# Optimization experiments

Hardware: AMD Instinct MI355X
Metric: run time of the kernel (lower is better)

Reference implementation:

```python
import jax, jax.numpy as jnp
import numpy as np

NUM_HEADS = 16


def setup_inputs() -> dict:
    key = jax.random.key(0)
    ks = jax.random.split(key, 4)
    B, C, T, D = 1, 1, 3072, 1024
    s = 1.0 / np.sqrt(D)
    return {
        "x": jax.random.normal(ks[0], (B, C, T, D), dtype=jnp.float32),
        "Wq": jax.random.normal(ks[1], (D, D), dtype=jnp.float32) * s,
        "bq": jnp.zeros((D,), dtype=jnp.float32),
        "Wk": jax.random.normal(ks[2], (D, D), dtype=jnp.float32) * s,
        "bk": jnp.zeros((D,), dtype=jnp.float32),
        "Wv": jax.random.normal(ks[3], (D, D), dtype=jnp.float32) * s,
        "bv": jnp.zeros((D,), dtype=jnp.float32),
        "gamma": jnp.float32(0.5),  # learned scalar; 0.0 at torch init, nonzero here for a meaningful signal
    }


def reference(x, Wq, bq, Wk, bk, Wv, bv, gamma):
    # x: (B, C, T, D); Linear acts on last dim (torch: y = x @ W.T + b)
    B, C, T, D = x.shape
    H = NUM_HEADS
    q = (jnp.einsum("bctd,ed->bcte", x, Wq) + bq).reshape(B, -1, T, H)  # (B, X, T, H), X = C*D/H
    k = (jnp.einsum("bctd,ed->bcte", x, Wk) + bk).reshape(B, -1, T, H)
    v = (jnp.einsum("bctd,ed->bcte", x, Wv) + bv).reshape(B, -1, T, H)
    q = q.transpose(0, 3, 2, 1)  # (B, H, T, X)
    k = k.transpose(0, 3, 1, 2)  # (B, H, X, T)
    energy = q @ k               # (B, H, T, T)  -- note: NO 1/sqrt(d) scaling, as in source
    attn = jax.nn.softmax(energy, axis=-1)
    v = v.transpose(0, 3, 2, 1)  # (B, H, T, X)
    out = attn @ v               # (B, H, T, X)
    out = out.transpose(0, 2, 3, 1).reshape(B, T, -1)  # (B, T, X*H) = (B, T, C*D)
    # residual broadcast: (B, T, C*D) + (B, C, T, D); valid since B == C == 1
    return gamma * out + x
```

## Files before the change

### kernel.cpp

```cpp
#include <hip/hip_runtime.h>


typedef _Float16 v8h __attribute__((ext_vector_type(8)));
typedef _Float16 v4h __attribute__((ext_vector_type(4)));
typedef float    v4f __attribute__((ext_vector_type(4)));

#define TSEQ 3072
#define DM   1024
#define NH   16
#define XD   64

__device__ __forceinline__ void async_load16(const void* g, void* l) {
  __builtin_amdgcn_global_load_lds(
      (const __attribute__((address_space(1))) unsigned int*)g,
      (__attribute__((address_space(3))) unsigned int*)l,
      16, 0, 0);
}

extern "C" __global__ __launch_bounds__(256) void cvt_kernel(
    const float* __restrict__ x, const float* __restrict__ wq,
    const float* __restrict__ wk, const float* __restrict__ wv,
    _Float16* __restrict__ xb, _Float16* __restrict__ wb)
{
  const int NX4 = (TSEQ * DM) / 4;
  const int NT  = NX4 * 2;
  for (int i = blockIdx.x * blockDim.x + threadIdx.x; i < NT;
       i += gridDim.x * blockDim.x) {
    float4 v;
    _Float16* dst;
    if (i < NX4) {
      v = ((const float4*)x)[i];
      dst = xb + (size_t)i * 4;
    } else {
      const int j = i - NX4;
      const int n = j >> 8;
      if (n < 1024)      v = ((const float4*)wq)[j];
      else if (n < 2048) v = ((const float4*)wk)[j - 262144];
      else               v = ((const float4*)wv)[j - 524288];
      dst = wb + (size_t)j * 4;
    }
    v4h h;
    h[0] = (_Float16)v.x; h[1] = (_Float16)v.y;
    h[2] = (_Float16)v.z; h[3] = (_Float16)v.w;
    *(v4h*)dst = h;
  }
}

extern "C" __global__ __launch_bounds__(256) void qkv_gemm_kernel(
    const _Float16* __restrict__ xb, const _Float16* __restrict__ wb,
    const float* __restrict__ bq, const float* __restrict__ bk,
    const float* __restrict__ bv,
    _Float16* __restrict__ qlin, _Float16* __restrict__ klin,
    _Float16* __restrict__ vlin)
{
  __shared__ _Float16 As[128 * 32];
  __shared__ _Float16 Bs[128 * 32];
  const int tid = threadIdx.x;
  const int w = tid >> 6, l = tid & 63;
  const int li = l & 15, lg = l >> 4;
  const int wm = w >> 1, wn = w & 1;
  const int m0 = blockIdx.y * 128, n0 = blockIdx.x * 128;
  v4f acc[4][4] = {};
  const int srow = l >> 2;
  const int scol = (l & 3) * 8;
  for (int k0 = 0; k0 < DM; k0 += 32) {
#pragma unroll
    for (int c = 0; c < 2; ++c) {
      const int rbase = c * 64 + w * 16;
      async_load16(xb + (size_t)(m0 + rbase + srow) * DM + k0 + scol, &As[rbase * 32]);
      async_load16(wb + (size_t)(n0 + rbase + srow) * DM + k0 + scol, &Bs[rbase * 32]);
    }
    __syncthreads();
    v8h af[4], bf[4];
#pragma unroll
    for (int mi = 0; mi < 4; ++mi)
      af[mi] = *(const v8h*)&As[(wm * 64 + mi * 16 + li) * 32 + lg * 8];
#pragma unroll
    for (int ni = 0; ni < 4; ++ni)
      bf[ni] = *(const v8h*)&Bs[(wn * 64 + ni * 16 + li) * 32 + lg * 8];
#pragma unroll
    for (int mi = 0; mi < 4; ++mi)
#pragma unroll
      for (int ni = 0; ni < 4; ++ni)
        acc[mi][ni] = __builtin_amdgcn_mfma_f32_16x16x32_f16(
            af[mi], bf[ni], acc[mi][ni], 0, 0, 0);
    __syncthreads();
  }
  const int which = n0 >> 10;
  const int ebase = n0 & 1023;
  const float* bias = which == 0 ? bq : (which == 1 ? bk : bv);
  _Float16* outp = which == 0 ? qlin : (which == 1 ? klin : vlin);
#pragma unroll
  for (int mi = 0; mi < 4; ++mi)
#pragma unroll
    for (int r = 0; r < 4; ++r) {
      const int t = m0 + wm * 64 + mi * 16 + lg * 4 + r;
#pragma unroll
      for (int ni = 0; ni < 4; ++ni) {
        const int e = ebase + wn * 64 + ni * 16 + li;
        outp[(size_t)t * DM + e] = (_Float16)(acc[mi][ni][r] + bias[e]);
      }
    }
}

extern "C" __global__ __launch_bounds__(256) void repack_kernel(
    const _Float16* __restrict__ qlin, const _Float16* __restrict__ klin,
    const _Float16* __restrict__ vlin,
    _Float16* __restrict__ qh, _Float16* __restrict__ kh,
    _Float16* __restrict__ vt)
{
  const int NE = NH * TSEQ * XD;
  for (int g = blockIdx.x * blockDim.x + threadIdx.x; g < 3 * NE;
       g += gridDim.x * blockDim.x) {
    if (g < 2 * NE) {
      const int gg = (g < NE) ? g : g - NE;
      const int xx = gg & 63;
      const int rest = gg >> 6;
      const int h = rest / TSEQ;
      const int i = rest - h * TSEQ;
      const int t = xx * 48 + (i >> 6);
      const int e = ((i & 63) << 4) + h;
      if (g < NE) qh[gg] = qlin[t * DM + e];
      else        kh[gg] = klin[t * DM + e];
    } else {
      const int o = g - 2 * NE;
      const int j = o % TSEQ;
      const int rest = o / TSEQ;
      const int xx = rest & 63;
      const int h = rest >> 6;
      const int t = xx * 48 + (j >> 6);
      const int e = ((j & 63) << 4) + h;
      vt[o] = vlin[t * DM + e];
    }
  }
}

extern "C" __global__ __launch_bounds__(256) void attn_kernel(
    const _Float16* __restrict__ qh, const _Float16* __restrict__ kh,
    const _Float16* __restrict__ vt, float* __restrict__ o_t)
{
  __shared__ _Float16 Ks[64 * 64];
  __shared__ _Float16 Vs[64 * 64];
  __shared__ _Float16 Ps[4][16 * 64];
  const int tid = threadIdx.x;
  const int w = tid >> 6, l = tid & 63;
  const int li = l & 15, lg = l >> 4;
  const int head = blockIdx.y;
  const int i0 = blockIdx.x * 64;
  const size_t hbase = (size_t)head * TSEQ * XD;

  v8h qf[2];
  {
    const _Float16* qrow = qh + hbase + (size_t)(i0 + w * 16 + li) * XD;
    qf[0] = *(const v8h*)(qrow + lg * 8);
    qf[1] = *(const v8h*)(qrow + 32 + lg * 8);
  }
  float mrun = -3.0e38f, lrun = 0.0f;
  v4f oacc[4] = {};

  for (int j0 = 0; j0 < TSEQ; j0 += 64) {
#pragma unroll
    for (int c = 0; c < 2; ++c) {
      const int rbase = c * 32 + w * 8;
      const int srow = rbase + (l >> 3);
      const int ss = ((l & 7) ^ (srow & 7)) * 8;
      async_load16(kh + hbase + (size_t)(j0 + srow) * XD + ss, &Ks[rbase * 64]);
      async_load16(vt + hbase + (size_t)srow * TSEQ + j0 + ss, &Vs[rbase * 64]);
    }
    __syncthreads();
    v4f e4[4];
#pragma unroll
    for (int kt = 0; kt < 4; ++kt) {
      v4f a = {};
#pragma unroll
      for (int xk = 0; xk < 2; ++xk) {
        v8h kf = *(const v8h*)&Ks[(kt * 16 + li) * 64 +
                                  ((xk * 4 + lg) ^ (li & 7)) * 8];
        a = __builtin_amdgcn_mfma_f32_16x16x32_f16(kf, qf[xk], a, 0, 0, 0);
      }
      e4[kt] = a;
    }
    float tm = -3.0e38f;
#pragma unroll
    for (int kt = 0; kt < 4; ++kt)
#pragma unroll
      for (int r = 0; r < 4; ++r) tm = fmaxf(tm, e4[kt][r]);
    tm = fmaxf(tm, __shfl_xor(tm, 16, 64));
    tm = fmaxf(tm, __shfl_xor(tm, 32, 64));
    const float mnew = fmaxf(mrun, tm);
    const float fsc = __expf(mrun - mnew);
    float ts = 0.0f;
    v4h pv[4];
#pragma unroll
    for (int kt = 0; kt < 4; ++kt)
#pragma unroll
      for (int r = 0; r < 4; ++r) {
        const float p = __expf(e4[kt][r] - mnew);
        ts += p;
        pv[kt][r] = (_Float16)p;
      }
    ts += __shfl_xor(ts, 16, 64);
    ts += __shfl_xor(ts, 32, 64);
    lrun = lrun * fsc + ts;
    mrun = mnew;
#pragma unroll
    for (int mi = 0; mi < 4; ++mi) oacc[mi] *= fsc;
#pragma unroll
    for (int kt = 0; kt < 4; ++kt) {
      const int ps = (kt * 2 + (lg >> 1)) ^ (li & 7);
      *(v4h*)&Ps[w][li * 64 + ps * 8 + (lg & 1) * 4] = pv[kt];
    }
#pragma unroll
    for (int jc = 0; jc < 2; ++jc) {
      v8h pf = *(const v8h*)&Ps[w][li * 64 + ((jc * 4 + lg) ^ (li & 7)) * 8];
#pragma unroll
      for (int mi = 0; mi < 4; ++mi) {
        v8h vf = *(const v8h*)&Vs[(mi * 16 + li) * 64 +
                                  ((jc * 4 + lg) ^ (li & 7)) * 8];
        oacc[mi] = __builtin_amdgcn_mfma_f32_16x16x32_f16(vf, pf, oacc[mi], 0, 0, 0);
      }
    }
    __syncthreads();
  }
  const float inv = 1.0f / lrun;
#pragma unroll
  for (int mi = 0; mi < 4; ++mi)
#pragma unroll
    for (int r = 0; r < 4; ++r) {
      const int xx = mi * 16 + lg * 4 + r;
      o_t[(size_t)(head * XD + xx) * TSEQ + i0 + w * 16 + li] = oacc[mi][r] * inv;
    }
}

extern "C" __global__ __launch_bounds__(256) void epilogue_kernel(
    const float* __restrict__ o_t, const float* __restrict__ xin,
    const float* __restrict__ gscal, float* __restrict__ outp)
{
  __shared__ __align__(16) float lds[64 * 260];
  const int tid = threadIdx.x;
  const int t0 = blockIdx.x * 64;
  const int d0 = blockIdx.y * 256;
  const int x0 = d0 >> 4;
#pragma unroll
  for (int pass = 0; pass < 16; ++pass) {
    const int p = pass * 16 + (tid >> 4);
    const int h = p & 15, xx = p >> 4;
    const int tf = (tid & 15) * 4;
    const float4 v = *(const float4*)(o_t + (size_t)(h * XD + x0 + xx) * TSEQ + t0 + tf);
    lds[(tf + 0) * 260 + p] = v.x;
    lds[(tf + 1) * 260 + p] = v.y;
    lds[(tf + 2) * 260 + p] = v.z;
    lds[(tf + 3) * 260 + p] = v.w;
  }
  __syncthreads();
  const float g = gscal[0];
  const int row = tid >> 2;
  const int cb = ((tid & 3) ^ (row & 3)) * 64;
  const int t = t0 + row;
#pragma unroll
  for (int c4 = 0; c4 < 64; c4 += 4) {
    const int c = cb + c4;
    const float4 xi = *(const float4*)(xin + (size_t)t * DM + d0 + c);
    const float4 ov = *(const float4*)&lds[row * 260 + c];
    float4 res;
    res.x = g * ov.x + xi.x;
    res.y = g * ov.y + xi.y;
    res.z = g * ov.z + xi.z;
    res.w = g * ov.w + xi.w;
    *(float4*)(outp + (size_t)t * DM + d0 + c) = res;
  }
}

extern "C" void kernel_launch(void* const* d_in, const int* in_sizes, int n_in,
                              void* d_out, int out_size, void* d_ws, size_t ws_size,
                              hipStream_t stream)
{
  const float* x  = (const float*)d_in[0];
  const float* Wq = (const float*)d_in[1];
  const float* bq = (const float*)d_in[2];
  const float* Wk = (const float*)d_in[3];
  const float* bk = (const float*)d_in[4];
  const float* Wv = (const float*)d_in[5];
  const float* bv = (const float*)d_in[6];
  const float* gm = (const float*)d_in[7];
  float* outp = (float*)d_out;
  char* ws = (char*)d_ws;
  const size_t SZH = (size_t)TSEQ * DM * sizeof(_Float16);
  _Float16* xb   = (_Float16*)(ws);
  _Float16* wb   = (_Float16*)(ws + SZH);
  _Float16* qlin = (_Float16*)(ws + 2 * SZH);
  _Float16* klin = (_Float16*)(ws + 3 * SZH);
  _Float16* vlin = (_Float16*)(ws + 4 * SZH);
  _Float16* qhp  = (_Float16*)(ws + 5 * SZH);
  _Float16* khp  = (_Float16*)(ws + 6 * SZH);
  _Float16* vtp  = (_Float16*)(ws + 7 * SZH);
  float*    o_t  = (float*)(ws);

  cvt_kernel<<<dim3(2048), dim3(256), 0, stream>>>(x, Wq, Wk, Wv, xb, wb);
  qkv_gemm_kernel<<<dim3(24, 24), dim3(256), 0, stream>>>(xb, wb, bq, bk, bv,
                                                          qlin, klin, vlin);
  repack_kernel<<<dim3(4096), dim3(256), 0, stream>>>(qlin, klin, vlin,
                                                      qhp, khp, vtp);
  attn_kernel<<<dim3(48, 16), dim3(256), 0, stream>>>(qhp, khp, vtp, o_t);
  epilogue_kernel<<<dim3(48, 4), dim3(256), 0, stream>>>(o_t, x, gm, outp);
  (void)in_sizes; (void)n_in; (void)out_size; (void)ws_size;
}
```

Baseline: 161.6 us.

## Rework attention pipeline: split-K waves, exp2 softmax, double-buffered GEMM, fp16 output

```diff
diff --git a/kernel.cpp b/kernel.cpp
--- a/kernel.cpp
+++ b/kernel.cpp
@@ -9,12 +9,20 @@
 #define DM   1024
 #define NH   16
 #define XD   64
+#define LOG2E 1.44269504f
 
 __device__ __forceinline__ void async_load16(const void* g, void* l) {
   __builtin_amdgcn_global_load_lds(
       (const __attribute__((address_space(1))) unsigned int*)g,
       (__attribute__((address_space(3))) unsigned int*)l,
       16, 0, 0);
+}
+
+__device__ __forceinline__ float fexp2(float x) {
+  float r; asm("v_exp_f32 %0, %1" : "=v"(r) : "v"(x)); return r;
+}
+__device__ __forceinline__ float flog2(float x) {
+  float r; asm("v_log_f32 %0, %1" : "=v"(r) : "v"(x)); return r;
 }
 
 extern "C" __global__ __launch_bounds__(256) void cvt_kernel(
@@ -53,31 +61,42 @@
     _Float16* __restrict__ qlin, _Float16* __restrict__ klin,
     _Float16* __restrict__ vlin)
 {
-  __shared__ _Float16 As[128 * 32];
-  __shared__ _Float16 Bs[128 * 32];
+  __shared__ _Float16 As[2][128 * 32];
+  __shared__ _Float16 Bs[2][128 * 32];
   const int tid = threadIdx.x;
   const int w = tid >> 6, l = tid & 63;
   const int li = l & 15, lg = l >> 4;
   const int wm = w >> 1, wn = w & 1;
-  const int m0 = blockIdx.y * 128, n0 = blockIdx.x * 128;
+  const int bid = blockIdx.x;
+  const int swz = (bid & 7) * 72 + (bid >> 3);
+  const int m0 = (swz / 24) * 128, n0 = (swz % 24) * 128;
   v4f acc[4][4] = {};
   const int srow = l >> 2;
   const int scol = (l & 3) * 8;
-  for (int k0 = 0; k0 < DM; k0 += 32) {
+
+  auto stage = [&](int buf, int k0) {
 #pragma unroll
     for (int c = 0; c < 2; ++c) {
       const int rbase = c * 64 + w * 16;
-      async_load16(xb + (size_t)(m0 + rbase + srow) * DM + k0 + scol, &As[rbase * 32]);
-      async_load16(wb + (size_t)(n0 + rbase + srow) * DM + k0 + scol, &Bs[rbase * 32]);
-    }
-    __syncthreads();
+      async_load16(xb + (size_t)(m0 + rbase + srow) * DM + k0 + scol,
+                   &As[buf][rbase * 32]);
+      async_load16(wb + (size_t)(n0 + rbase + srow) * DM + k0 + scol,
+                   &Bs[buf][rbase * 32]);
+    }
+  };
+
+  stage(0, 0);
+  __syncthreads();
+  for (int kt = 0; kt < DM / 32; ++kt) {
+    const int buf = kt & 1;
+    if (kt + 1 < DM / 32) stage(buf ^ 1, (kt + 1) * 32);
     v8h af[4], bf[4];
 #pragma unroll
     for (int mi = 0; mi < 4; ++mi)
-      af[mi] = *(const v8h*)&As[(wm * 64 + mi * 16 + li) * 32 + lg * 8];
+      af[mi] = *(const v8h*)&As[buf][(wm * 64 + mi * 16 + li) * 32 + lg * 8];
 #pragma unroll
     for (int ni = 0; ni < 4; ++ni)
-      bf[ni] = *(const v8h*)&Bs[(wn * 64 + ni * 16 + li) * 32 + lg * 8];
+      bf[ni] = *(const v8h*)&Bs[buf][(wn * 64 + ni * 16 + li) * 32 + lg * 8];
 #pragma unroll
     for (int mi = 0; mi < 4; ++mi)
 #pragma unroll
@@ -104,26 +123,22 @@
 }
 
 extern "C" __global__ __launch_bounds__(256) void repack_kernel(
-    const _Float16* __restrict__ qlin, const _Float16* __restrict__ klin,
-    const _Float16* __restrict__ vlin,
-    _Float16* __restrict__ qh, _Float16* __restrict__ kh,
-    _Float16* __restrict__ vt)
+    const _Float16* __restrict__ klin, const _Float16* __restrict__ vlin,
+    _Float16* __restrict__ kh, _Float16* __restrict__ vt)
 {
   const int NE = NH * TSEQ * XD;
-  for (int g = blockIdx.x * blockDim.x + threadIdx.x; g < 3 * NE;
+  for (int g = blockIdx.x * blockDim.x + threadIdx.x; g < 2 * NE;
        g += gridDim.x * blockDim.x) {
-    if (g < 2 * NE) {
-      const int gg = (g < NE) ? g : g - NE;
-      const int xx = gg & 63;
-      const int rest = gg >> 6;
+    if (g < NE) {
+      const int xx = g & 63;
+      const int rest = g >> 6;
       const int h = rest / TSEQ;
-      const int i = rest - h * TSEQ;
-      const int t = xx * 48 + (i >> 6);
-      const int e = ((i & 63) << 4) + h;
-      if (g < NE) qh[gg] = qlin[t * DM + e];
-      else        kh[gg] = klin[t * DM + e];
+      const int j = rest - h * TSEQ;
+      const int t = xx * 48 + (j >> 6);
+      const int e = ((j & 63) << 4) + h;
+      kh[g] = (_Float16)((float)klin[t * DM + e] * LOG2E);
     } else {
-      const int o = g - 2 * NE;
+      const int o = g - NE;
       const int j = o % TSEQ;
       const int rest = o / TSEQ;
       const int xx = rest & 63;
@@ -136,138 +151,200 @@
 }
 
 extern "C" __global__ __launch_bounds__(256) void attn_kernel(
-    const _Float16* __restrict__ qh, const _Float16* __restrict__ kh,
-    const _Float16* __restrict__ vt, float* __restrict__ o_t)
-{
-  __shared__ _Float16 Ks[64 * 64];
-  __shared__ _Float16 Vs[64 * 64];
-  __shared__ _Float16 Ps[4][16 * 64];
+    const _Float16* __restrict__ qlin, const _Float16* __restrict__ kh,
+    const _Float16* __restrict__ vt, _Float16* __restrict__ pOut)
+{
+  __shared__ _Float16 SH[16384];
+  __shared__ float sml[4][64];
   const int tid = threadIdx.x;
   const int w = tid >> 6, l = tid & 63;
   const int li = l & 15, lg = l >> 4;
   const int head = blockIdx.y;
   const int i0 = blockIdx.x * 64;
-  const size_t hbase = (size_t)head * TSEQ * XD;
-
-  v8h qf[2];
+  const size_t hb = (size_t)head * TSEQ * XD;
+
+  v8h qf[4][2];
+#pragma unroll
+  for (int ct = 0; ct < 4; ++ct) {
+    const int i = i0 + ct * 16 + li;
+    const int tbase = i >> 6;
+    const int ecol = ((i & 63) << 4) + head;
+#pragma unroll
+    for (int xk = 0; xk < 2; ++xk)
+#pragma unroll
+      for (int e = 0; e < 8; ++e) {
+        const int x = xk * 32 + lg * 8 + e;
+        qf[ct][xk][e] = qlin[(size_t)(x * 48 + tbase) * DM + ecol];
+      }
+  }
+
+  v4f oacc[4][4] = {};
+  float m2[4], l4[4];
+#pragma unroll
+  for (int ct = 0; ct < 4; ++ct) { m2[ct] = 24.0f * LOG2E; l4[ct] = 0.0f; }
+
+  const int r8 = l >> 3, c8 = l & 7;
+
+  auto stage = [&](int buf, int j0) {
+#pragma unroll
+    for (int s = 0; s < 2; ++s) {
+      const int n = w * 2 + s;
+      const int row = n * 8 + r8;
+      async_load16(kh + hb + (size_t)(j0 + row) * XD + ((c8 ^ (row & 7)) * 8),
+                   SH + buf * 8192 + n * 512);
+      async_load16(vt + hb + (size_t)row * TSEQ + j0 + ((c8 ^ (row & 7)) * 8),
+                   SH + buf * 8192 + 4096 + n * 512);
+    }
+  };
+
+  stage(0, 0);
+  __syncthreads();
+
+  const int krow = w * 16 + li;
+  const int kc0 = ((0 + lg) ^ (krow & 7)) * 8;
+  const int kc1 = ((4 + lg) ^ (krow & 7)) * 8;
+
+  for (int it = 0; it < TSEQ / 64; ++it) {
+    const int buf = it & 1;
+    if (it + 1 < TSEQ / 64) stage(buf ^ 1, (it + 1) * 64);
+    const _Float16* Kc = SH + buf * 8192;
+    const _Float16* Vc = SH + buf * 8192 + 4096;
+
+    const v8h kf0 = *(const v8h*)&Kc[krow * 64 + kc0];
+    const v8h kf1 = *(const v8h*)&Kc[krow * 64 + kc1];
+    v4f e4[4];
+#pragma unroll
+    for (int ct = 0; ct < 4; ++ct) {
+      v4f a = {};
+      a = __builtin_amdgcn_mfma_f32_16x16x32_f16(kf0, qf[ct][0], a, 0, 0, 0);
+      a = __builtin_amdgcn_mfma_f32_16x16x32_f16(kf1, qf[ct][1], a, 0, 0, 0);
+      e4[ct] = a;
+    }
+    float p[4][4];
+#pragma unroll
+    for (int ct = 0; ct < 4; ++ct)
+#pragma unroll
+      for (int r = 0; r < 4; ++r) p[ct][r] = fexp2(e4[ct][r] - m2[ct]);
+    float gmx = fmaxf(fmaxf(fmaxf(e4[0][0], e4[0][1]), fmaxf(e4[0][2], e4[0][3])),
+                      fmaxf(fmaxf(e4[1][0], e4[1][1]), fmaxf(e4[1][2], e4[1][3])));
+    gmx = fmaxf(gmx,
+          fmaxf(fmaxf(fmaxf(e4[2][0], e4[2][1]), fmaxf(e4[2][2], e4[2][3])),
+                fmaxf(fmaxf(e4[3][0], e4[3][1]), fmaxf(e4[3][2], e4[3][3]))));
+    const float mmn = fminf(fminf(m2[0], m2[1]), fminf(m2[2], m2[3]));
+    if (__any(gmx > mmn + 11.5f)) {
+#pragma unroll
+      for (int ct = 0; ct < 4; ++ct) {
+        float tm = fmaxf(fmaxf(e4[ct][0], e4[ct][1]), fmaxf(e4[ct][2], e4[ct][3]));
+        tm = fmaxf(tm, __shfl_xor(tm, 16, 64));
+        tm = fmaxf(tm, __shfl_xor(tm, 32, 64));
+        if (tm > m2[ct]) {
+          const float fs = fexp2(m2[ct] - tm);
+#pragma unroll
+          for (int r = 0; r < 4; ++r) p[ct][r] *= fs;
+          l4[ct] *= fs;
+#pragma unroll
+          for (int mi = 0; mi < 4; ++mi) oacc[mi][ct] *= fs;
+          m2[ct] = tm;
+        }
+      }
+    }
+    v4h pv[4];
+#pragma unroll
+    for (int ct = 0; ct < 4; ++ct) {
+      l4[ct] += (p[ct][0] + p[ct][1]) + (p[ct][2] + p[ct][3]);
+#pragma unroll
+      for (int r = 0; r < 4; ++r) pv[ct][r] = (_Float16)p[ct][r];
+    }
+#pragma unroll
+    for (int mi = 0; mi < 4; ++mi) {
+      const int vrow = mi * 16 + li;
+      const v4h vf = *(const v4h*)&Vc[vrow * 64 +
+                        (((w * 2 + (lg >> 1)) ^ (vrow & 7)) * 8) + (lg & 1) * 4];
+#pragma unroll
+      for (int ct = 0; ct < 4; ++ct)
+        oacc[mi][ct] = __builtin_amdgcn_mfma_f32_16x16x16f16(
+            vf, pv[ct], oacc[mi][ct], 0, 0, 0);
+    }
+    __syncthreads();
+  }
+
+  _Float16* on = SH;
+#pragma unroll
+  for (int ct = 0; ct < 4; ++ct) {
+    float ls = l4[ct];
+    ls += __shfl_xor(ls, 16, 64);
+    ls += __shfl_xor(ls, 32, 64);
+    const float inv = 1.0f / ls;
+    if (lg == 0) sml[w][ct * 16 + li] = m2[ct] + flog2(ls);
+#pragma unroll
+    for (int mi = 0; mi < 4; ++mi) {
+      v4h o4;
+#pragma unroll
+      for (int r = 0; r < 4; ++r) o4[r] = (_Float16)(oacc[mi][ct][r] * inv);
+      *(v4h*)&on[w * 4096 + (ct * 16 + li) * 64 + mi * 16 + lg * 4] = o4;
+    }
+  }
+  __syncthreads();
   {
-    const _Float16* qrow = qh + hbase + (size_t)(i0 + w * 16 + li) * XD;
-    qf[0] = *(const v8h*)(qrow + lg * 8);
-    qf[1] = *(const v8h*)(qrow + 32 + lg * 8);
-  }
-  float mrun = -3.0e38f, lrun = 0.0f;
-  v4f oacc[4] = {};
-
-  for (int j0 = 0; j0 < TSEQ; j0 += 64) {
-#pragma unroll
-    for (int c = 0; c < 2; ++c) {
-      const int rbase = c * 32 + w * 8;
-      const int srow = rbase + (l >> 3);
-      const int ss = ((l & 7) ^ (srow & 7)) * 8;
-      async_load16(kh + hbase + (size_t)(j0 + srow) * XD + ss, &Ks[rbase * 64]);
-      async_load16(vt + hbase + (size_t)srow * TSEQ + j0 + ss, &Vs[rbase * 64]);
-    }
-    __syncthreads();
-    v4f e4[4];
-#pragma unroll
-    for (int kt = 0; kt < 4; ++kt) {
-      v4f a = {};
-#pragma unroll
-      for (int xk = 0; xk < 2; ++xk) {
-        v8h kf = *(const v8h*)&Ks[(kt * 16 + li) * 64 +
-                                  ((xk * 4 + lg) ^ (li & 7)) * 8];
-        a = __builtin_amdgcn_mfma_f32_16x16x32_f16(kf, qf[xk], a, 0, 0, 0);
+    const int im = w * 16 + (l >> 2);
+    const int xs = (l & 3) * 16;
+    float s0 = sml[0][im], s1 = sml[1][im], s2 = sml[2][im], s3 = sml[3][im];
+    const float M = fmaxf(fmaxf(s0, s1), fmaxf(s2, s3));
+    float u[4];
+    u[0] = fexp2(s0 - M); u[1] = fexp2(s1 - M);
+    u[2] = fexp2(s2 - M); u[3] = fexp2(s3 - M);
+    const float D = u[0] + u[1] + u[2] + u[3];
+    float acc[16] = {};
+#pragma unroll
+    for (int sw = 0; sw < 4; ++sw) {
+      const v8h a = *(const v8h*)&on[sw * 4096 + im * 64 + xs];
+      const v8h b = *(const v8h*)&on[sw * 4096 + im * 64 + xs + 8];
+#pragma unroll
+      for (int e = 0; e < 8; ++e) {
+        acc[e]     += u[sw] * (float)a[e];
+        acc[8 + e] += u[sw] * (float)b[e];
       }
-      e4[kt] = a;
-    }
-    float tm = -3.0e38f;
-#pragma unroll
-    for (int kt = 0; kt < 4; ++kt)
-#pragma unroll
-      for (int r = 0; r < 4; ++r) tm = fmaxf(tm, e4[kt][r]);
-    tm = fmaxf(tm, __shfl_xor(tm, 16, 64));
-    tm = fmaxf(tm, __shfl_xor(tm, 32, 64));
-    const float mnew = fmaxf(mrun, tm);
-    const float fsc = __expf(mrun - mnew);
-    float ts = 0.0f;
-    v4h pv[4];
-#pragma unroll
-    for (int kt = 0; kt < 4; ++kt)
-#pragma unroll
-      for (int r = 0; r < 4; ++r) {
-        const float p = __expf(e4[kt][r] - mnew);
-        ts += p;
-        pv[kt][r] = (_Float16)p;
-      }
-    ts += __shfl_xor(ts, 16, 64);
-    ts += __shfl_xor(ts, 32, 64);
-    lrun = lrun * fsc + ts;
-    mrun = mnew;
-#pragma unroll
-    for (int mi = 0; mi < 4; ++mi) oacc[mi] *= fsc;
-#pragma unroll
-    for (int kt = 0; kt < 4; ++kt) {
-      const int ps = (kt * 2 + (lg >> 1)) ^ (li & 7);
-      *(v4h*)&Ps[w][li * 64 + ps * 8 + (lg & 1) * 4] = pv[kt];
-    }
-#pragma unroll
-    for (int jc = 0; jc < 2; ++jc) {
-      v8h pf = *(const v8h*)&Ps[w][li * 64 + ((jc * 4 + lg) ^ (li & 7)) * 8];
-#pragma unroll
-      for (int mi = 0; mi < 4; ++mi) {
-        v8h vf = *(const v8h*)&Vs[(mi * 16 + li) * 64 +
-                                  ((jc * 4 + lg) ^ (li & 7)) * 8];
-        oacc[mi] = __builtin_amdgcn_mfma_f32_16x16x32_f16(vf, pf, oacc[mi], 0, 0, 0);
-      }
-    }
-    __syncthreads();
-  }
-  const float inv = 1.0f / lrun;
-#pragma unroll
-  for (int mi = 0; mi < 4; ++mi)
-#pragma unroll
-    for (int r = 0; r < 4; ++r) {
-      const int xx = mi * 16 + lg * 4 + r;
-      o_t[(size_t)(head * XD + xx) * TSEQ + i0 + w * 16 + li] = oacc[mi][r] * inv;
-    }
+    }
+    const float di = 1.0f / D;
+    v8h r0, r1;
+#pragma unroll
+    for (int e = 0; e < 8; ++e) {
+      r0[e] = (_Float16)(acc[e] * di);
+      r1[e] = (_Float16)(acc[8 + e] * di);
+    }
+    _Float16* dst = pOut + (size_t)(i0 + im) * DM + head * 64 + xs;
+    *(v8h*)dst = r0;
+    *(v8h*)(dst + 8) = r1;
+  }
 }
 
 extern "C" __global__ __launch_bounds__(256) void epilogue_kernel(
-    const float* __restrict__ o_t, const float* __restrict__ xin,
+    const _Float16* __restrict__ pO, const float* __restrict__ xin,
     const float* __restrict__ gscal, float* __restrict__ outp)
 {
-  __shared__ __align__(16) float lds[64 * 260];
+  __shared__ _Float16 po[8 * 1024];
   const int tid = threadIdx.x;
-  const int t0 = blockIdx.x * 64;
-  const int d0 = blockIdx.y * 256;
-  const int x0 = d0 >> 4;
-#pragma unroll
-  for (int pass = 0; pass < 16; ++pass) {
-    const int p = pass * 16 + (tid >> 4);
-    const int h = p & 15, xx = p >> 4;
-    const int tf = (tid & 15) * 4;
-    const float4 v = *(const float4*)(o_t + (size_t)(h * XD + x0 + xx) * TSEQ + t0 + tf);
-    lds[(tf + 0) * 260 + p] = v.x;
-    lds[(tf + 1) * 260 + p] = v.y;
-    lds[(tf + 2) * 260 + p] = v.z;
-    lds[(tf + 3) * 260 + p] = v.w;
+  const size_t t0 = (size_t)blockIdx.x * 8;
+  {
+    const _Float16* src = pO + t0 * DM + tid * 32;
+    v8h* d = (v8h*)&po[tid * 32];
+#pragma unroll
+    for (int c = 0; c < 4; ++c) d[c] = *(const v8h*)(src + c * 8);
   }
   __syncthreads();
   const float g = gscal[0];
-  const int row = tid >> 2;
-  const int cb = ((tid & 3) ^ (row & 3)) * 64;
-  const int t = t0 + row;
-#pragma unroll
-  for (int c4 = 0; c4 < 64; c4 += 4) {
-    const int c = cb + c4;
-    const float4 xi = *(const float4*)(xin + (size_t)t * DM + d0 + c);
-    const float4 ov = *(const float4*)&lds[row * 260 + c];
-    float4 res;
-    res.x = g * ov.x + xi.x;
-    res.y = g * ov.y + xi.y;
-    res.z = g * ov.z + xi.z;
-    res.w = g * ov.w + xi.w;
-    *(float4*)(outp + (size_t)t * DM + d0 + c) = res;
+  const int tr = tid >> 5;
+  const int d0 = (tid & 31) * 32;
+  const size_t rb = (t0 + tr) * DM + d0;
+#pragma unroll
+  for (int c4 = 0; c4 < 8; ++c4) {
+    const float4 xi = *(const float4*)&xin[rb + c4 * 4];
+    float4 r;
+    r.x = g * (float)po[tr * 1024 + ((c4 * 4 + 0) & 15) * 64 + ((d0 + c4 * 4 + 0) >> 4)] + xi.x;
+    r.y = g * (float)po[tr * 1024 + ((c4 * 4 + 1) & 15) * 64 + ((d0 + c4 * 4 + 1) >> 4)] + xi.y;
+    r.z = g * (float)po[tr * 1024 + ((c4 * 4 + 2) & 15) * 64 + ((d0 + c4 * 4 + 2) >> 4)] + xi.z;
+    r.w = g * (float)po[tr * 1024 + ((c4 * 4 + 3) & 15) * 64 + ((d0 + c4 * 4 + 3) >> 4)] + xi.w;
+    *(float4*)&outp[rb + c4 * 4] = r;
   }
 }
 
@@ -291,17 +368,15 @@
   _Float16* qlin = (_Float16*)(ws + 2 * SZH);
   _Float16* klin = (_Float16*)(ws + 3 * SZH);
   _Float16* vlin = (_Float16*)(ws + 4 * SZH);
-  _Float16* qhp  = (_Float16*)(ws + 5 * SZH);
-  _Float16* khp  = (_Float16*)(ws + 6 * SZH);
-  _Float16* vtp  = (_Float16*)(ws + 7 * SZH);
-  float*    o_t  = (float*)(ws);
-
-  cvt_kernel<<<dim3(2048), dim3(256), 0, stream>>>(x, Wq, Wk, Wv, xb, wb);
-  qkv_gemm_kernel<<<dim3(24, 24), dim3(256), 0, stream>>>(xb, wb, bq, bk, bv,
-                                                          qlin, klin, vlin);
-  repack_kernel<<<dim3(4096), dim3(256), 0, stream>>>(qlin, klin, vlin,
-                                                      qhp, khp, vtp);
-  attn_kernel<<<dim3(48, 16), dim3(256), 0, stream>>>(qhp, khp, vtp, o_t);
-  epilogue_kernel<<<dim3(48, 4), dim3(256), 0, stream>>>(o_t, x, gm, outp);
+  _Float16* khp  = (_Float16*)(ws + 5 * SZH);
+  _Float16* vtp  = (_Float16*)(ws + 6 * SZH);
+  _Float16* pO   = (_Float16*)(ws + 7 * SZH);
+
+  cvt_kernel<<<dim3(1024), dim3(256), 0, stream>>>(x, Wq, Wk, Wv, xb, wb);
+  qkv_gemm_kernel<<<dim3(576), dim3(256), 0, stream>>>(xb, wb, bq, bk, bv,
+                                                       qlin, klin, vlin);
+  repack_kernel<<<dim3(2048), dim3(256), 0, stream>>>(klin, vlin, khp, vtp);
+  attn_kernel<<<dim3(48, 16), dim3(256), 0, stream>>>(qlin, khp, vtp, pO);
+  epilogue_kernel<<<dim3(384), dim3(256), 0, stream>>>(pO, x, gm, outp);
   (void)in_sizes; (void)n_in; (void)out_size; (void)ws_size;
 }
```

Measured after the change: 234.0 us. +44.8%, slower.

## Rework attention softmax with exp2, lazy rescaling, register P, and fp16 output layout

Applied to the files above, without the earlier changes.

```diff
diff --git a/kernel.cpp b/kernel.cpp
--- a/kernel.cpp
+++ b/kernel.cpp
@@ -9,12 +9,17 @@
 #define DM   1024
 #define NH   16
 #define XD   64
+#define LOG2E 1.44269504f
 
 __device__ __forceinline__ void async_load16(const void* g, void* l) {
   __builtin_amdgcn_global_load_lds(
       (const __attribute__((address_space(1))) unsigned int*)g,
       (__attribute__((address_space(3))) unsigned int*)l,
       16, 0, 0);
+}
+
+__device__ __forceinline__ float fexp2(float x) {
+  float r; asm("v_exp_f32 %0, %1" : "=v"(r) : "v"(x)); return r;
 }
 
 extern "C" __global__ __launch_bounds__(256) void cvt_kernel(
@@ -59,7 +64,9 @@
   const int w = tid >> 6, l = tid & 63;
   const int li = l & 15, lg = l >> 4;
   const int wm = w >> 1, wn = w & 1;
-  const int m0 = blockIdx.y * 128, n0 = blockIdx.x * 128;
+  const int bid = blockIdx.x;
+  const int swz = (bid & 7) * 72 + (bid >> 3);
+  const int m0 = (swz / 24) * 128, n0 = (swz % 24) * 128;
   v4f acc[4][4] = {};
   const int srow = l >> 2;
   const int scol = (l & 3) * 8;
@@ -121,7 +128,7 @@
       const int t = xx * 48 + (i >> 6);
       const int e = ((i & 63) << 4) + h;
       if (g < NE) qh[gg] = qlin[t * DM + e];
-      else        kh[gg] = klin[t * DM + e];
+      else        kh[gg] = (_Float16)((float)klin[t * DM + e] * LOG2E);
     } else {
       const int o = g - 2 * NE;
       const int j = o % TSEQ;
@@ -137,137 +144,144 @@
 
 extern "C" __global__ __launch_bounds__(256) void attn_kernel(
     const _Float16* __restrict__ qh, const _Float16* __restrict__ kh,
-    const _Float16* __restrict__ vt, float* __restrict__ o_t)
+    const _Float16* __restrict__ vt, _Float16* __restrict__ pOut)
 {
   __shared__ _Float16 Ks[64 * 64];
   __shared__ _Float16 Vs[64 * 64];
-  __shared__ _Float16 Ps[4][16 * 64];
   const int tid = threadIdx.x;
   const int w = tid >> 6, l = tid & 63;
   const int li = l & 15, lg = l >> 4;
   const int head = blockIdx.y;
   const int i0 = blockIdx.x * 64;
-  const size_t hbase = (size_t)head * TSEQ * XD;
-
-  v8h qf[2];
+  const size_t hb = (size_t)head * TSEQ * XD;
+
+  v8h qf0, qf1;
   {
-    const _Float16* qrow = qh + hbase + (size_t)(i0 + w * 16 + li) * XD;
-    qf[0] = *(const v8h*)(qrow + lg * 8);
-    qf[1] = *(const v8h*)(qrow + 32 + lg * 8);
-  }
-  float mrun = -3.0e38f, lrun = 0.0f;
+    const _Float16* qrow = qh + hb + (size_t)(i0 + w * 16 + li) * XD;
+    qf0 = *(const v8h*)(qrow + lg * 8);
+    qf1 = *(const v8h*)(qrow + 32 + lg * 8);
+  }
+  float m2 = 24.0f * LOG2E;
+  float l4 = 0.0f;
   v4f oacc[4] = {};
+  const int r8 = l >> 3, c8 = l & 7;
 
   for (int j0 = 0; j0 < TSEQ; j0 += 64) {
 #pragma unroll
-    for (int c = 0; c < 2; ++c) {
-      const int rbase = c * 32 + w * 8;
-      const int srow = rbase + (l >> 3);
-      const int ss = ((l & 7) ^ (srow & 7)) * 8;
-      async_load16(kh + hbase + (size_t)(j0 + srow) * XD + ss, &Ks[rbase * 64]);
-      async_load16(vt + hbase + (size_t)srow * TSEQ + j0 + ss, &Vs[rbase * 64]);
+    for (int s = 0; s < 2; ++s) {
+      const int n = w * 2 + s;
+      const int row = n * 8 + r8;
+      async_load16(kh + hb + (size_t)(j0 + row) * XD + ((c8 ^ (row & 7)) * 8),
+                   Ks + n * 512);
+      async_load16(vt + hb + (size_t)row * TSEQ + j0 + ((c8 ^ (row & 7)) * 8),
+                   Vs + n * 512);
     }
     __syncthreads();
+
     v4f e4[4];
 #pragma unroll
     for (int kt = 0; kt < 4; ++kt) {
+      const int krow = kt * 16 + li;
+      const v8h kf0 = *(const v8h*)&Ks[krow * 64 + ((lg ^ (krow & 7)) * 8)];
+      const v8h kf1 = *(const v8h*)&Ks[krow * 64 + (((4 + lg) ^ (krow & 7)) * 8)];
       v4f a = {};
-#pragma unroll
-      for (int xk = 0; xk < 2; ++xk) {
-        v8h kf = *(const v8h*)&Ks[(kt * 16 + li) * 64 +
-                                  ((xk * 4 + lg) ^ (li & 7)) * 8];
-        a = __builtin_amdgcn_mfma_f32_16x16x32_f16(kf, qf[xk], a, 0, 0, 0);
+      a = __builtin_amdgcn_mfma_f32_16x16x32_f16(kf0, qf0, a, 0, 0, 0);
+      a = __builtin_amdgcn_mfma_f32_16x16x32_f16(kf1, qf1, a, 0, 0, 0);
+      e4[kt] = a;
+    }
+
+    float p[4][4];
+#pragma unroll
+    for (int kt = 0; kt < 4; ++kt)
+#pragma unroll
+      for (int r = 0; r < 4; ++r) p[kt][r] = fexp2(e4[kt][r] - m2);
+
+    float lmax = fmaxf(fmaxf(fmaxf(e4[0][0], e4[0][1]), fmaxf(e4[0][2], e4[0][3])),
+                       fmaxf(fmaxf(e4[1][0], e4[1][1]), fmaxf(e4[1][2], e4[1][3])));
+    lmax = fmaxf(lmax,
+           fmaxf(fmaxf(fmaxf(e4[2][0], e4[2][1]), fmaxf(e4[2][2], e4[2][3])),
+                 fmaxf(fmaxf(e4[3][0], e4[3][1]), fmaxf(e4[3][2], e4[3][3]))));
+    if (__any(lmax > m2 + 11.5f)) {
+      float rm = lmax;
+      rm = fmaxf(rm, __shfl_xor(rm, 16, 64));
+      rm = fmaxf(rm, __shfl_xor(rm, 32, 64));
+      const float fs = (rm > m2) ? fexp2(m2 - rm) : 1.0f;
+#pragma unroll
+      for (int kt = 0; kt < 4; ++kt)
+#pragma unroll
+        for (int r = 0; r < 4; ++r) p[kt][r] *= fs;
+      l4 *= fs;
+#pragma unroll
+      for (int mi = 0; mi < 4; ++mi) oacc[mi] *= fs;
+      m2 = fmaxf(m2, rm);
+    }
+
+    v4h pv[4];
+#pragma unroll
+    for (int kt = 0; kt < 4; ++kt)
+#pragma unroll
+      for (int r = 0; r < 4; ++r) pv[kt][r] = (_Float16)p[kt][r];
+    l4 += ((p[0][0] + p[0][1]) + (p[0][2] + p[0][3]))
+        + ((p[1][0] + p[1][1]) + (p[1][2] + p[1][3]))
+        + ((p[2][0] + p[2][1]) + (p[2][2] + p[2][3]))
+        + ((p[3][0] + p[3][1]) + (p[3][2] + p[3][3]));
+
+#pragma unroll
+    for (int mi = 0; mi < 4; ++mi) {
+      const int vrow = mi * 16 + li;
+      const int vb = vrow * 64 + (lg & 1) * 4;
+      v4f a = oacc[mi];
+#pragma unroll
+      for (int kt = 0; kt < 4; ++kt) {
+        const v4h vf = *(const v4h*)&Vs[vb + (((kt * 2 + (lg >> 1)) ^ (vrow & 7)) * 8)];
+        a = __builtin_amdgcn_mfma_f32_16x16x16f16(vf, pv[kt], a, 0, 0, 0);
       }
-      e4[kt] = a;
-    }
-    float tm = -3.0e38f;
-#pragma unroll
-    for (int kt = 0; kt < 4; ++kt)
-#pragma unroll
-      for (int r = 0; r < 4; ++r) tm = fmaxf(tm, e4[kt][r]);
-    tm = fmaxf(tm, __shfl_xor(tm, 16, 64));
-    tm = fmaxf(tm, __shfl_xor(tm, 32, 64));
-    const float mnew = fmaxf(mrun, tm);
-    const float fsc = __expf(mrun - mnew);
-    float ts = 0.0f;
-    v4h pv[4];
-#pragma unroll
-    for (int kt = 0; kt < 4; ++kt)
-#pragma unroll
-      for (int r = 0; r < 4; ++r) {
-        const float p = __expf(e4[kt][r] - mnew);
-        ts += p;
-        pv[kt][r] = (_Float16)p;
-      }
-    ts += __shfl_xor(ts, 16, 64);
-    ts += __shfl_xor(ts, 32, 64);
-    lrun = lrun * fsc + ts;
-    mrun = mnew;
-#pragma unroll
-    for (int mi = 0; mi < 4; ++mi) oacc[mi] *= fsc;
-#pragma unroll
-    for (int kt = 0; kt < 4; ++kt) {
-      const int ps = (kt * 2 + (lg >> 1)) ^ (li & 7);
-      *(v4h*)&Ps[w][li * 64 + ps * 8 + (lg & 1) * 4] = pv[kt];
-    }
-#pragma unroll
-    for (int jc = 0; jc < 2; ++jc) {
-      v8h pf = *(const v8h*)&Ps[w][li * 64 + ((jc * 4 + lg) ^ (li & 7)) * 8];
-#pragma unroll
-      for (int mi = 0; mi < 4; ++mi) {
-        v8h vf = *(const v8h*)&Vs[(mi * 16 + li) * 64 +
-                                  ((jc * 4 + lg) ^ (li & 7)) * 8];
-        oacc[mi] = __builtin_amdgcn_mfma_f32_16x16x32_f16(vf, pf, oacc[mi], 0, 0, 0);
-      }
+      oacc[mi] = a;
     }
     __syncthreads();
   }
-  const float inv = 1.0f / lrun;
-#pragma unroll
-  for (int mi = 0; mi < 4; ++mi)
-#pragma unroll
-    for (int r = 0; r < 4; ++r) {
-      const int xx = mi * 16 + lg * 4 + r;
-      o_t[(size_t)(head * XD + xx) * TSEQ + i0 + w * 16 + li] = oacc[mi][r] * inv;
-    }
+
+  float ls = l4;
+  ls += __shfl_xor(ls, 16, 64);
+  ls += __shfl_xor(ls, 32, 64);
+  const float inv = 1.0f / ls;
+  const int irow = i0 + w * 16 + li;
+#pragma unroll
+  for (int mi = 0; mi < 4; ++mi) {
+    v4h o4;
+#pragma unroll
+    for (int r = 0; r < 4; ++r) o4[r] = (_Float16)(oacc[mi][r] * inv);
+    *(v4h*)&pOut[(size_t)irow * DM + head * 64 + mi * 16 + lg * 4] = o4;
+  }
 }
 
 extern "C" __global__ __launch_bounds__(256) void epilogue_kernel(
-    const float* __restrict__ o_t, const float* __restrict__ xin,
+    const _Float16* __restrict__ pO, const float* __restrict__ xin,
     const float* __restrict__ gscal, float* __restrict__ outp)
 {
-  __shared__ __align__(16) float lds[64 * 260];
+  __shared__ _Float16 po[8 * 1024];
   const int tid = threadIdx.x;
-  const int t0 = blockIdx.x * 64;
-  const int d0 = blockIdx.y * 256;
-  const int x0 = d0 >> 4;
-#pragma unroll
-  for (int pass = 0; pass < 16; ++pass) {
-    const int p = pass * 16 + (tid >> 4);
-    const int h = p & 15, xx = p >> 4;
-    const int tf = (tid & 15) * 4;
-    const float4 v = *(const float4*)(o_t + (size_t)(h * XD + x0 + xx) * TSEQ + t0 + tf);
-    lds[(tf + 0) * 260 + p] = v.x;
-    lds[(tf + 1) * 260 + p] = v.y;
-    lds[(tf + 2) * 260 + p] = v.z;
-    lds[(tf + 3) * 260 + p] = v.w;
+  const size_t t0 = (size_t)blockIdx.x * 8;
+  {
+    const _Float16* src = pO + t0 * DM + tid * 32;
+    v8h* d = (v8h*)&po[tid * 32];
+#pragma unroll
+    for (int c = 0; c < 4; ++c) d[c] = *(const v8h*)(src + c * 8);
   }
   __syncthreads();
   const float g = gscal[0];
-  const int row = tid >> 2;
-  const int cb = ((tid & 3) ^ (row & 3)) * 64;
-  const int t = t0 + row;
-#pragma unroll
-  for (int c4 = 0; c4 < 64; c4 += 4) {
-    const int c = cb + c4;
-    const float4 xi = *(const float4*)(xin + (size_t)t * DM + d0 + c);
-    const float4 ov = *(const float4*)&lds[row * 260 + c];
-    float4 res;
-    res.x = g * ov.x + xi.x;
-    res.y = g * ov.y + xi.y;
-    res.z = g * ov.z + xi.z;
-    res.w = g * ov.w + xi.w;
-    *(float4*)(outp + (size_t)t * DM + d0 + c) = res;
+  const int tr = tid >> 5;
+  const int d0 = (tid & 31) * 32;
+  const size_t rb = (t0 + tr) * DM + d0;
+#pragma unroll
+  for (int c4 = 0; c4 < 8; ++c4) {
+    const float4 xi = *(const float4*)&xin[rb + c4 * 4];
+    float4 r;
+    r.x = g * (float)po[tr * 1024 + ((c4 * 4 + 0) & 15) * 64 + ((d0 + c4 * 4 + 0) >> 4)] + xi.x;
+    r.y = g * (float)po[tr * 1024 + ((c4 * 4 + 1) & 15) * 64 + ((d0 + c4 * 4 + 1) >> 4)] + xi.y;
+    r.z = g * (float)po[tr * 1024 + ((c4 * 4 + 2) & 15) * 64 + ((d0 + c4 * 4 + 2) >> 4)] + xi.z;
+    r.w = g * (float)po[tr * 1024 + ((c4 * 4 + 3) & 15) * 64 + ((d0 + c4 * 4 + 3) >> 4)] + xi.w;
+    *(float4*)&outp[rb + c4 * 4] = r;
   }
 }
 
@@ -294,14 +308,14 @@
   _Float16* qhp  = (_Float16*)(ws + 5 * SZH);
   _Float16* khp  = (_Float16*)(ws + 6 * SZH);
   _Float16* vtp  = (_Float16*)(ws + 7 * SZH);
-  float*    o_t  = (float*)(ws);
-
-  cvt_kernel<<<dim3(2048), dim3(256), 0, stream>>>(x, Wq, Wk, Wv, xb, wb);
-  qkv_gemm_kernel<<<dim3(24, 24), dim3(256), 0, stream>>>(xb, wb, bq, bk, bv,
-                                                          qlin, klin, vlin);
+  _Float16* pO   = (_Float16*)(ws);
+
+  cvt_kernel<<<dim3(1024), dim3(256), 0, stream>>>(x, Wq, Wk, Wv, xb, wb);
+  qkv_gemm_kernel<<<dim3(576), dim3(256), 0, stream>>>(xb, wb, bq, bk, bv,
+                                                       qlin, klin, vlin);
   repack_kernel<<<dim3(4096), dim3(256), 0, stream>>>(qlin, klin, vlin,
                                                       qhp, khp, vtp);
-  attn_kernel<<<dim3(48, 16), dim3(256), 0, stream>>>(qhp, khp, vtp, o_t);
-  epilogue_kernel<<<dim3(48, 4), dim3(256), 0, stream>>>(o_t, x, gm, outp);
+  attn_kernel<<<dim3(48, 16), dim3(256), 0, stream>>>(qhp, khp, vtp, pO);
+  epilogue_kernel<<<dim3(384), dim3(256), 0, stream>>>(pO, x, gm, outp);
   (void)in_sizes; (void)n_in; (void)out_size; (void)ws_size;
 }
```

Measured after the change: 152.7 us. -5.5%, faster.
